# Kernel optimization log

Hardware: AMD Instinct MI355X
Metric: run time of the kernel (lower is better)

## Reference

```python
import jax, jax.numpy as jnp
import numpy as np

X_DIM = 64
Y_DIM = 64
U_DIM = 64
BATCH = 32
SEQ_LEN = 2048
DT = 1.0 / 1024.0
EPS = 1e-4


def setup_inputs() -> dict:
    key = jax.random.key(0)
    k_y, k_a, k_c = jax.random.split(key, 3)
    y = jax.random.normal(k_y, (BATCH, SEQ_LEN, Y_DIM), dtype=jnp.float32)
    # parameters, matching the module's initialization (small noise added to A/C for generality)
    A = jnp.diag(-0.01 * (jnp.arange(X_DIM, dtype=jnp.float32) + 1.0)) \
        + 0.001 * jax.random.normal(k_a, (X_DIM, X_DIM), dtype=jnp.float32)
    B = jnp.eye(X_DIM, U_DIM, dtype=jnp.float32) * 0.1
    C = 0.1 * jax.random.normal(k_c, (Y_DIM, X_DIM), dtype=jnp.float32)
    L_Q = jnp.eye(X_DIM, dtype=jnp.float32) * 0.316
    L_R = jnp.eye(U_DIM, dtype=jnp.float32) * 0.316
    L_V = jnp.eye(Y_DIM, dtype=jnp.float32)
    L_Q_proc = jnp.eye(X_DIM, dtype=jnp.float32) * 0.1
    x0_mean = jnp.zeros((X_DIM,), dtype=jnp.float32)
    P0 = jnp.eye(X_DIM, dtype=jnp.float32) * 0.1
    return {"y": y, "A": A, "B": B, "C": C, "L_Q": L_Q, "L_R": L_R,
            "L_V": L_V, "L_Q_proc": L_Q_proc, "x0_mean": x0_mean, "P0": P0}


def _riccati_step(S, H, n):
    # Euler step of the augmented Hamiltonian flow; P = V @ U^{-1}
    S_new = S + DT * (H @ S)
    U, V = S_new[:n], S_new[n:]
    X = V @ jnp.linalg.inv(U)
    return X, S_new


def _forward(y, A, B, C, L_Q, L_R, L_V, L_Q_proc, x0_mean, P0):
    n = A.shape[0]
    u_dim = B.shape[1]
    y_dim = C.shape[0]
    batch, seq_len, _ = y.shape

    Q = L_Q @ L_Q.T
    R = L_R @ L_R.T
    V = L_V @ L_V.T
    Q_proc = L_Q_proc @ L_Q_proc.T

    # normalize observations (torch.std is unbiased -> ddof=1)
    y_mean = y.mean(axis=(0, 1), keepdims=True)
    y_std = y.std(axis=(0, 1), keepdims=True, ddof=1)
    yn = (y - y_mean) / (y_std + EPS)

    # --- LQR Riccati recursion: P_seq, K_seq (sequential scan over time) ---
    R_inv_reg = jnp.linalg.inv(R + EPS * jnp.eye(u_dim, dtype=R.dtype))
    H_care = jnp.block([[A, -B @ jnp.linalg.inv(R) @ B.T],
                        [-Q, -A.T]])  # augmented Hamiltonian (2n, 2n)

    def lqr_step(S, _):
        X, S_new = _riccati_step(S, H_care, n)
        P = 0.5 * (X + X.T)
        K = R_inv_reg @ (B.T @ P)  # (u_dim, n)
        return S_new, (P, K)

    S0 = jnp.concatenate([jnp.eye(n, dtype=Q.dtype), Q], axis=0)  # P0 = Q
    _, (P_seq, K_seq) = jax.lax.scan(lqr_step, S0, None, length=seq_len)

    # --- Kalman filter (sequential scan, data-dependent per-step linear algebra) ---
    V_reg = V + EPS * jnp.eye(y_dim, dtype=V.dtype)
    V_chol = jnp.linalg.cholesky(V_reg)
    log_det_V = 2.0 * jnp.sum(jnp.log(jnp.diagonal(V_chol)))
    Z = jnp.zeros((n, n), dtype=A.dtype)
    LOG_2PI = jnp.log(2.0 * jnp.pi).astype(A.dtype)

    def kf_step(carry, inp):
        x_t, S, ll = carry
        K_t, y_t = inp  # (u_dim, n), (batch, y_dim)
        A_eff = A - B @ K_t
        x_pred = x_t + DT * (x_t @ A_eff.T)  # (batch, n)
        H_t = jnp.block([[A_eff, Q_proc], [Z, -A_eff.T]])
        P_new, S = _riccati_step(S, H_t, n)
        P_pred = 0.5 * (P_new + P_new.T)
        residual = y_t - x_pred @ C.T  # (batch, y_dim)
        CtP = C @ P_pred  # (y_dim, n)
        Sm = CtP @ C.T + V
        S_inv = jnp.linalg.inv(Sm + EPS * jnp.eye(y_dim, dtype=Sm.dtype))
        Kg = CtP.T @ S_inv  # (n, y_dim)
        x_new = x_pred + residual @ Kg.T
        quad = jnp.sum(residual * (residual @ S_inv.T))  # sum_b r^T S_inv r
        ll = ll - 0.5 * (quad + log_det_V + y_dim * LOG_2PI)
        return (x_new, S, ll), x_new

    S0_kf = jnp.concatenate([jnp.eye(n, dtype=P0.dtype), P0], axis=0)
    x0 = jnp.broadcast_to(x0_mean, (batch, n))
    y_t_major = jnp.swapaxes(yn, 0, 1)  # (T, B, y_dim)
    (_, _, ll), x_filt_t = jax.lax.scan(kf_step, (x0, S0_kf, jnp.float32(0.0)),
                                        (K_seq, y_t_major))
    x_filt = jnp.swapaxes(x_filt_t, 0, 1)  # (B, T, n)
    log_likelihood = ll / seq_len

    # controls, prediction, quadratic costs (fully vectorized)
    u_seq = -jnp.einsum('tux,btx->btu', K_seq, x_filt)
    y_pred = x_filt @ C.T
    x_cost = jnp.einsum('btx,xz,btz->b', x_filt, Q, x_filt)
    u_cost = jnp.einsum('btu,uv,btv->b', u_seq, R, u_seq)
    control_cost = jnp.mean(x_cost + u_cost)
    return log_likelihood, control_cost, x_filt, u_seq, y_pred, yn


def reference(y, A, B, C, L_Q, L_R, L_V, L_Q_proc, x0_mean, P0):
    return _forward(y, A, B, C, L_Q, L_R, L_V, L_Q_proc, x0_mean, P0)
```

## Files before the change

### kernel.cpp

```cpp
#include <hip/hip_runtime.h>
#include <math.h>

#define XD 64
#define SEQL 2048
#define NB 32
#define DT_C  (1.0f/1024.0f)
#define EPS_C 1e-4f
#define LD 68
#define LOG2PI 1.8378770664093453f
#define CHUNK 8
#define NCH 256

#define OFF_PARTIAL 0u
#define OFF_MEAN    32768u
#define OFF_STD     32832u
#define OFF_Q       32896u
#define OFF_R       36992u
#define OFF_VM      41088u
#define OFF_QP      45184u
#define OFF_RIREG   49280u
#define OFF_LOGDET  53376u
#define OFF_CHAIN   53440u
#define OFF_POW     250048u
#define OFF_BOUNDS  1298624u
#define OFF_K       1568960u
#define OFF_AEFF    9957568u
#define OFF_UV      18346176u
#define OFF_G       35123392u
#define OFF_B       43512000u
#define OFF_OPS2    OFF_UV
#define OFF_OPS3G   47706304u
#define OFF_OPS3B   49803456u
#define OFF_SB2     50852032u
#define OFF_XB      52949184u
#define OFF_QUAD    53473472u
#define OFF_COST    53475520u
#define OFF_BRI     53541056u

#define OOFF_XF 2
#define OOFF_U  4194306
#define OOFF_YP 8388610
#define OOFF_YN 12582914

template<int KD>
__device__ __forceinline__ void mmNN(int t, float* __restrict__ out, int ldo,
    const float* __restrict__ A, int lda, const float* __restrict__ B, int ldb,
    const float* __restrict__ addC = nullptr, int ldc = 0, float alpha = 1.0f)
{
  const int r0 = (t >> 4) << 2, c0 = (t & 15) << 2;
  float acc[4][4] = {};
  for (int k = 0; k < KD; k += 4) {
    float a_[4][4];
    #pragma unroll
    for (int i = 0; i < 4; ++i) {
      const float4 x = *(const float4*)&A[(r0+i)*lda + k];
      a_[i][0]=x.x; a_[i][1]=x.y; a_[i][2]=x.z; a_[i][3]=x.w;
    }
    #pragma unroll
    for (int kk = 0; kk < 4; ++kk) {
      const float4 bv = *(const float4*)&B[(k+kk)*ldb + c0];
      #pragma unroll
      for (int i = 0; i < 4; ++i) {
        const float a = a_[i][kk];
        acc[i][0] += a*bv.x; acc[i][1] += a*bv.y; acc[i][2] += a*bv.z; acc[i][3] += a*bv.w;
      }
    }
  }
  #pragma unroll
  for (int i = 0; i < 4; ++i)
    #pragma unroll
    for (int j = 0; j < 4; ++j) {
      float v = alpha*acc[i][j];
      if (addC) v += addC[(r0+i)*ldc + (c0+j)];
      out[(r0+i)*ldo + (c0+j)] = v;
    }
}

template<int KD>
__device__ __forceinline__ void mmTA(int t, float* __restrict__ out, int ldo,
    const float* __restrict__ A, int lda, const float* __restrict__ B, int ldb,
    const float* __restrict__ addC = nullptr, int ldc = 0, float alpha = 1.0f)
{
  const int r0 = (t >> 4) << 2, c0 = (t & 15) << 2;
  float acc[4][4] = {};
  for (int k = 0; k < KD; k += 4) {
    #pragma unroll
    for (int kk = 0; kk < 4; ++kk) {
      const float4 av4 = *(const float4*)&A[(k+kk)*lda + r0];
      const float4 bv4 = *(const float4*)&B[(k+kk)*ldb + c0];
      const float av[4] = {av4.x, av4.y, av4.z, av4.w};
      const float bv[4] = {bv4.x, bv4.y, bv4.z, bv4.w};
      #pragma unroll
      for (int i = 0; i < 4; ++i)
        #pragma unroll
        for (int j = 0; j < 4; ++j)
          acc[i][j] += av[i]*bv[j];
    }
  }
  #pragma unroll
  for (int i = 0; i < 4; ++i)
    #pragma unroll
    for (int j = 0; j < 4; ++j) {
      float v = alpha*acc[i][j];
      if (addC) v += addC[(r0+i)*ldc + (c0+j)];
      out[(r0+i)*ldo + (c0+j)] = v;
    }
}

template<int KD>
__device__ __forceinline__ void mmTB(int t, float* __restrict__ out, int ldo,
    const float* __restrict__ A, int lda, const float* __restrict__ B, int ldb,
    const float* __restrict__ addC = nullptr, int ldc = 0, float alpha = 1.0f)
{
  const int r0 = (t >> 4) << 2, c0 = (t & 15) << 2;
  float acc[4][4] = {};
  for (int k = 0; k < KD; k += 4) {
    float a_[4][4], b_[4][4];
    #pragma unroll
    for (int i = 0; i < 4; ++i) {
      const float4 x = *(const float4*)&A[(r0+i)*lda + k];
      a_[i][0]=x.x; a_[i][1]=x.y; a_[i][2]=x.z; a_[i][3]=x.w;
    }
    #pragma unroll
    for (int j = 0; j < 4; ++j) {
      const float4 x = *(const float4*)&B[(c0+j)*ldb + k];
      b_[j][0]=x.x; b_[j][1]=x.y; b_[j][2]=x.z; b_[j][3]=x.w;
    }
    #pragma unroll
    for (int i = 0; i < 4; ++i)
      #pragma unroll
      for (int j = 0; j < 4; ++j)
        acc[i][j] += a_[i][0]*b_[j][0] + a_[i][1]*b_[j][1] + a_[i][2]*b_[j][2] + a_[i][3]*b_[j][3];
  }
  #pragma unroll
  for (int i = 0; i < 4; ++i)
    #pragma unroll
    for (int j = 0; j < 4; ++j) {
      float v = alpha*acc[i][j];
      if (addC) v += addC[(r0+i)*ldc + (c0+j)];
      out[(r0+i)*ldo + (c0+j)] = v;
    }
}

__device__ __forceinline__ void symTile(int t, float* __restrict__ outb, const float* __restrict__ X)
{
  const int r0 = (t >> 4) << 2, c0 = (t & 15) << 2;
  float xa[4][4], xb[4][4];
  #pragma unroll
  for (int i = 0; i < 4; ++i) {
    const float4 u = *(const float4*)&X[(r0+i)*LD + c0];
    xa[i][0]=u.x; xa[i][1]=u.y; xa[i][2]=u.z; xa[i][3]=u.w;
    const float4 v = *(const float4*)&X[(c0+i)*LD + r0];
    xb[i][0]=v.x; xb[i][1]=v.y; xb[i][2]=v.z; xb[i][3]=v.w;
  }
  #pragma unroll
  for (int i = 0; i < 4; ++i) {
    float4 o;
    o.x = 0.5f*(xa[i][0] + xb[0][i]);
    o.y = 0.5f*(xa[i][1] + xb[1][i]);
    o.z = 0.5f*(xa[i][2] + xb[2][i]);
    o.w = 0.5f*(xa[i][3] + xb[3][i]);
    *(float4*)&outb[(r0+i)*LD + c0] = o;
  }
}

template<int KD>
__device__ __forceinline__ void mm32NN(int t, float* __restrict__ out, int ldo,
    const float* __restrict__ A, int lda, const float* __restrict__ B, int ldb,
    const float* __restrict__ addC = nullptr, int ldc = 0, float alpha = 1.0f)
{
  const int r0 = (t >> 4) << 1, c0 = (t & 15) << 2;
  float acc[2][4] = {};
  for (int k = 0; k < KD; k += 4) {
    float a_[2][4];
    #pragma unroll
    for (int i = 0; i < 2; ++i) {
      const float4 x = *(const float4*)&A[(r0+i)*lda + k];
      a_[i][0]=x.x; a_[i][1]=x.y; a_[i][2]=x.z; a_[i][3]=x.w;
    }
    #pragma unroll
    for (int kk = 0; kk < 4; ++kk) {
      const float4 bv = *(const float4*)&B[(k+kk)*ldb + c0];
      #pragma unroll
      for (int i = 0; i < 2; ++i) {
        const float a = a_[i][kk];
        acc[i][0] += a*bv.x; acc[i][1] += a*bv.y; acc[i][2] += a*bv.z; acc[i][3] += a*bv.w;
      }
    }
  }
  #pragma unroll
  for (int i = 0; i < 2; ++i)
    #pragma unroll
    for (int j = 0; j < 4; ++j) {
      float v = alpha*acc[i][j];
      if (addC) v += addC[(r0+i)*ldc + (c0+j)];
      out[(r0+i)*ldo + (c0+j)] = v;
    }
}

template<int KD>
__device__ __forceinline__ void mm32TB(int t, float* __restrict__ out, int ldo,
    const float* __restrict__ A, size_t lda, const float* __restrict__ B, int ldb,
    const float* __restrict__ addC = nullptr, size_t ldc = 0, float alpha = 1.0f)
{
  const int r0 = (t >> 4) << 1, c0 = (t & 15) << 2;
  float acc[2][4] = {};
  for (int k = 0; k < KD; k += 4) {
    float a_[2][4], b_[4][4];
    #pragma unroll
    for (int i = 0; i < 2; ++i) {
      const float4 x = *(const float4*)&A[(size_t)(r0+i)*lda + k];
      a_[i][0]=x.x; a_[i][1]=x.y; a_[i][2]=x.z; a_[i][3]=x.w;
    }
    #pragma unroll
    for (int j = 0; j < 4; ++j) {
      const float4 x = *(const float4*)&B[(c0+j)*ldb + k];
      b_[j][0]=x.x; b_[j][1]=x.y; b_[j][2]=x.z; b_[j][3]=x.w;
    }
    #pragma unroll
    for (int i = 0; i < 2; ++i)
      #pragma unroll
      for (int j = 0; j < 4; ++j)
        acc[i][j] += a_[i][0]*b_[j][0] + a_[i][1]*b_[j][1] + a_[i][2]*b_[j][2] + a_[i][3]*b_[j][3];
  }
  #pragma unroll
  for (int i = 0; i < 2; ++i)
    #pragma unroll
    for (int j = 0; j < 4; ++j) {
      float v = alpha*acc[i][j];
      if (addC) v += addC[(size_t)(r0+i)*ldc + (c0+j)];
      out[(r0+i)*ldo + (c0+j)] = v;
    }
}

__device__ __forceinline__ void gj64(int t, float* __restrict__ Am, float* __restrict__ R)
{
  const int r = t >> 2;
  const int c0 = (t & 3) << 4;
  for (int k = 0; k < 64; ++k) {
    __syncthreads();
    const float pv = Am[k*LD + k];
    const float f = Am[r*LD + k] / pv;
    if (r != k) {
      #pragma unroll
      for (int c = 0; c < 16; c += 4) {
        float4 ak = *(const float4*)&Am[k*LD + c0 + c];
        float4 ar = *(float4*)&Am[r*LD + c0 + c];
        ar.x -= f*ak.x; ar.y -= f*ak.y; ar.z -= f*ak.z; ar.w -= f*ak.w;
        *(float4*)&Am[r*LD + c0 + c] = ar;
        float4 rk = *(const float4*)&R[k*LD + c0 + c];
        float4 rr = *(float4*)&R[r*LD + c0 + c];
        rr.x -= f*rk.x; rr.y -= f*rk.y; rr.z -= f*rk.z; rr.w -= f*rk.w;
        *(float4*)&R[r*LD + c0 + c] = rr;
      }
    }
  }
  __syncthreads();
  const float dinv = 1.0f / Am[r*LD + r];
  #pragma unroll
  for (int c = 0; c < 16; c += 4) {
    float4 rr = *(float4*)&R[r*LD + c0 + c];
    rr.x *= dinv; rr.y *= dinv; rr.z *= dinv; rr.w *= dinv;
    *(float4*)&R[r*LD + c0 + c] = rr;
  }
  __syncthreads();
}

__device__ __forceinline__ void gji8(int t, float* __restrict__ Am)
{
  const int r  = t >> 2;
  const int c0 = (t & 3) << 4;
  const int pj = (t >> 4) & 7;
  const int c4 = (t & 15) << 2;
  const int lane = t & 63;
  const int li = lane >> 3, lj = lane & 7;
  for (int kb = 0; kb < 8; ++kb) {
    const int K = kb << 3;
    __syncthreads();
    const bool inK = ((unsigned)(r - K)) < 8u;
    float4 f0 = make_float4(0.f,0.f,0.f,0.f), f1 = f0;
    if (!inK) {
      f0 = *(const float4*)&Am[r*LD + K];
      f1 = *(const float4*)&Am[r*LD + K + 4];
    }
    float a = Am[(K+li)*LD + K + lj];
    float w = (li == lj) ? 1.0f : 0.0f;
    #pragma unroll
    for (int p = 0; p < 8; ++p) {
      const float pv  = __shfl(a, p*8 + p, 64);
      const float pvr = __builtin_amdgcn_rcpf(pv);
      const float aip = __shfl(a, li*8 + p, 64);
      const float apj = __shfl(a, p*8 + lj, 64);
      const float wpj = __shfl(w, p*8 + lj, 64);
      const float fi  = aip * pvr;
      if (li == p) { a *= pvr; w *= pvr; }
      else         { a -= fi * apj; w -= fi * wpj; }
    }
    float wrow[8];
    #pragma unroll
    for (int m = 0; m < 8; ++m) wrow[m] = __shfl(w, pj*8 + m, 64);
    float4 acc = make_float4(0.f,0.f,0.f,0.f);
    if (t < 128) {
      #pragma unroll
      for (int m = 0; m < 8; ++m) {
        const float4 rv = *(const float4*)&Am[(K+m)*LD + c4];
        acc.x += wrow[m]*rv.x; acc.y += wrow[m]*rv.y; acc.z += wrow[m]*rv.z; acc.w += wrow[m]*rv.w;
      }
      const unsigned dp = (unsigned)(c4 - K);
      if (dp < 8u) acc = make_float4(wrow[dp], wrow[dp+1], wrow[dp+2], wrow[dp+3]);
    }
    __syncthreads();
    if (t < 128) *(float4*)&Am[(K+pj)*LD + c4] = acc;
    __syncthreads();
    if (!inK) {
      const float fj[8] = {f0.x, f0.y, f0.z, f0.w, f1.x, f1.y, f1.z, f1.w};
      #pragma unroll
      for (int c = 0; c < 16; c += 4) {
        const int cab = c0 + c;
        const bool isPiv = ((unsigned)(cab - K)) < 8u;
        float4 v = isPiv ? make_float4(0.f,0.f,0.f,0.f) : *(float4*)&Am[r*LD + cab];
        #pragma unroll
        for (int j = 0; j < 8; ++j) {
          const float4 p4 = *(const float4*)&Am[(K+j)*LD + cab];
          v.x -= fj[j]*p4.x; v.y -= fj[j]*p4.y; v.z -= fj[j]*p4.z; v.w -= fj[j]*p4.w;
        }
        *(float4*)&Am[r*LD + cab] = v;
      }
    }
  }
  __syncthreads();
}


__global__ __launch_bounds__(256) void k_stats(const float* __restrict__ y, float* __restrict__ ws)
{
  __shared__ float sbuf[4][128];
  const int t = threadIdx.x, blk = blockIdx.x;
  const int d = t & 63, g = t >> 6;
  float s = 0.f, s2 = 0.f;
  for (int r = g; r < 256; r += 4) {
    const float v = y[(size_t)(blk*256 + r)*64 + d];
    s += v; s2 += v*v;
  }
  sbuf[g][d] = s; sbuf[g][64+d] = s2;
  __syncthreads();
  if (t < 128) ws[OFF_PARTIAL + (size_t)blk*128 + t] = sbuf[0][t]+sbuf[1][t]+sbuf[2][t]+sbuf[3][t];
}

__global__ __launch_bounds__(256) void k_setup(
    const float* __restrict__ A, const float* __restrict__ Bi,
    const float* __restrict__ LQ, const float* __restrict__ LR,
    const float* __restrict__ LV, const float* __restrict__ LQp,
    float* __restrict__ ws)
{
  __shared__ float b1[64*LD], b2[64*LD], b3[64*LD], b4[64*LD], bQ[64*LD];
  __shared__ float sred[128];
  const int t = threadIdx.x;

  if (t < 128) {
    float acc = 0.f;
    for (int p = 0; p < 256; ++p) acc += ws[OFF_PARTIAL + (size_t)p*128 + t];
    sred[t] = acc;
  }
  __syncthreads();
  if (t < 64) {
    const float mean = sred[t] * (1.0f/65536.0f);
    const float var = (sred[64+t] - 65536.0f*mean*mean) * (1.0f/65535.0f);
    ws[OFF_MEAN + t] = mean;
    ws[OFF_STD + t] = sqrtf(var);
  }

  mmTB<64>(t, bQ, LD, LQ, 64, LQ, 64);
  mmTB<64>(t, b3, LD, LR, 64, LR, 64);
  mmTB<64>(t, ws+OFF_VM, 64, LV, 64, LV, 64);
  mmTB<64>(t, ws+OFF_QP, 64, LQp, 64, LQp, 64);
  __syncthreads();
  for (int idx = t; idx < 4096; idx += 256) {
    const int r = idx>>6, c = idx&63;
    ws[OFF_Q + idx] = bQ[r*LD+c];
    ws[OFF_R + idx] = b3[r*LD+c];
    b1[r*LD+c] = b3[r*LD+c] + ((r==c)?EPS_C:0.f);
    b2[r*LD+c] = (r==c)?1.f:0.f;
  }
  gj64(t, b1, b2);
  mmNN<64>(t, b4, LD, Bi, 64, b2, LD);
  __syncthreads();
  for (int idx = t; idx < 4096; idx += 256) {
    ws[OFF_RIREG + idx] = b2[(idx>>6)*LD+(idx&63)];
    ws[OFF_BRI + idx]   = b4[(idx>>6)*LD+(idx&63)];
  }
  __syncthreads();
  for (int idx = t; idx < 4096; idx += 256) {
    const int r = idx>>6, c = idx&63;
    b1[r*LD+c] = b3[r*LD+c];
    b2[r*LD+c] = (r==c)?1.f:0.f;
  }
  gj64(t, b1, b2);
  mmTB<64>(t, b3, LD, b2, LD, Bi, 64);
  __syncthreads();
  mmNN<64>(t, b4, LD, Bi, 64, b3, LD);
  mmTB<64>(t, b1, LD, LV, 64, LV, 64);
  __syncthreads();
  if (t < 64) b1[t*LD+t] += EPS_C;
  {
    const int r = t >> 2, c0 = (t & 3) << 4;
    float lsum = 0.f;
    for (int k = 0; k < 64; ++k) {
      __syncthreads();
      const float pv = b1[k*LD+k];
      lsum += logf(pv);
      const float f = b1[r*LD+k] / pv;
      if (r != k) {
        #pragma unroll
        for (int c = 0; c < 16; c += 4) {
          float4 ak = *(const float4*)&b1[k*LD+c0+c];
          float4 ar = *(float4*)&b1[r*LD+c0+c];
          ar.x -= f*ak.x; ar.y -= f*ak.y; ar.z -= f*ak.z; ar.w -= f*ak.w;
          *(float4*)&b1[r*LD+c0+c] = ar;
        }
      }
    }
    if (t == 0) ws[OFF_LOGDET] = lsum;
  }
  __syncthreads();
  float* M0 = ws + OFF_CHAIN;
  for (int idx = t; idx < 16384; idx += 256) {
    const int i = idx >> 7, j = idx & 127;
    float v;
    if (i < 64) v = (j < 64) ? (((i==j)?1.f:0.f) + DT_C*A[i*64+j]) : (-DT_C*b4[i*LD + (j-64)]);
    else        v = (j < 64) ? (-DT_C*bQ[(i-64)*LD + j]) : (((i==j)?1.f:0.f) - DT_C*A[(j-64)*64 + (i-64)]);
    M0[idx] = v;
  }
  for (int idx = t; idx < 16384; idx += 256) {
    const int i = idx >> 7, j = idx & 127;
    ws[OFF_POW + idx] = (i==j)?1.f:0.f;
  }
  for (int idx = t; idx < 8192; idx += 256) {
    const int i = idx >> 6, j = idx & 63;
    ws[OFF_BOUNDS + idx] = (i < 64) ? ((i==j)?1.f:0.f) : bQ[(i-64)*LD + j];
  }
}

__global__ __launch_bounds__(256) void k_yn(const float* __restrict__ y, const float* __restrict__ ws, float* __restrict__ out)
{
  const size_t i0 = ((size_t)blockIdx.x*256 + threadIdx.x)*4;
  const int d = (int)(i0 & 63);
  const float4 v = *(const float4*)&y[i0];
  const float4 m = *(const float4*)&ws[OFF_MEAN + d];
  const float4 s = *(const float4*)&ws[OFF_STD + d];
  float* o = out + OOFF_YN + i0;
  o[0] = (v.x - m.x)/(s.x + EPS_C);
  o[1] = (v.y - m.y)/(s.y + EPS_C);
  o[2] = (v.z - m.z)/(s.z + EPS_C);
  o[3] = (v.w - m.w)/(s.w + EPS_C);
}

__global__ __launch_bounds__(256) void k_sq(const float* __restrict__ src, float* __restrict__ dst)
{
  const int t = threadIdx.x;
  const int r = blockIdx.x*8 + (t >> 5);
  const int c0 = (t & 31) << 2;
  float acc[4] = {0.f,0.f,0.f,0.f};
  for (int k = 0; k < 128; k += 4) {
    const float4 a4 = *(const float4*)&src[r*128 + k];
    const float av[4] = {a4.x, a4.y, a4.z, a4.w};
    #pragma unroll
    for (int kk = 0; kk < 4; ++kk) {
      const float4 bv = *(const float4*)&src[(k+kk)*128 + c0];
      acc[0] += av[kk]*bv.x; acc[1] += av[kk]*bv.y; acc[2] += av[kk]*bv.z; acc[3] += av[kk]*bv.w;
    }
  }
  float4 o; o.x=acc[0]; o.y=acc[1]; o.z=acc[2]; o.w=acc[3];
  *(float4*)&dst[r*128 + c0] = o;
}

__global__ __launch_bounds__(256) void k_powbounds(const float* __restrict__ chain, float* __restrict__ ws, int level)
{
  const int nbp = 4 << level;
  const int t = threadIdx.x;
  if ((int)blockIdx.x < nbp) {
    const float* chainj = chain + (size_t)level*16384;
    float* powt = ws + OFF_POW;
    const int i = blockIdx.x >> 2, sub = blockIdx.x & 3;
    const float* Bm = powt + (size_t)i*16384;
    float* D = powt + (size_t)(i + (1<<level))*16384;
    const int r0 = sub*32 + ((t >> 4) << 1);
    const int c0 = (t & 15) << 3;
    float acc[2][8] = {};
    for (int k = 0; k < 128; k += 4) {
      float a_[2][4];
      {
        const float4 x = *(const float4*)&chainj[r0*128 + k];
        a_[0][0]=x.x; a_[0][1]=x.y; a_[0][2]=x.z; a_[0][3]=x.w;
        const float4 y2 = *(const float4*)&chainj[(r0+1)*128 + k];
        a_[1][0]=y2.x; a_[1][1]=y2.y; a_[1][2]=y2.z; a_[1][3]=y2.w;
      }
      #pragma unroll
      for (int kk = 0; kk < 4; ++kk) {
        const float4 b0 = *(const float4*)&Bm[(k+kk)*128 + c0];
        const float4 b1v = *(const float4*)&Bm[(k+kk)*128 + c0 + 4];
        #pragma unroll
        for (int i2 = 0; i2 < 2; ++i2) {
          const float a = a_[i2][kk];
          acc[i2][0] += a*b0.x; acc[i2][1] += a*b0.y; acc[i2][2] += a*b0.z; acc[i2][3] += a*b0.w;
          acc[i2][4] += a*b1v.x; acc[i2][5] += a*b1v.y; acc[i2][6] += a*b1v.z; acc[i2][7] += a*b1v.w;
        }
      }
    }
    #pragma unroll
    for (int i2 = 0; i2 < 2; ++i2)
      #pragma unroll
      for (int j = 0; j < 8; ++j)
        D[(r0+i2)*128 + c0 + j] = acc[i2][j];
  } else {
    const int bb = blockIdx.x - nbp;
    const int kb = bb >> 1, sub = bb & 1;
    const int dsti = kb + (1 << level);
    if (dsti > 32) return;
    const float* chainp = chain + (size_t)(6+level)*16384;
    const float* S = ws + OFF_BOUNDS + (size_t)kb*8192;
    float* D = ws + OFF_BOUNDS + (size_t)dsti*8192;
    const int r0 = sub*64 + ((t >> 4) << 2);
    const int c0 = (t & 15) << 2;
    float acc[4][4] = {};
    for (int k = 0; k < 128; k += 4) {
      float a_[4][4];
      #pragma unroll
      for (int i = 0; i < 4; ++i) {
        const float4 x = *(const float4*)&chainp[(r0+i)*128 + k];
        a_[i][0]=x.x; a_[i][1]=x.y; a_[i][2]=x.z; a_[i][3]=x.w;
      }
      #pragma unroll
      for (int kk = 0; kk < 4; ++kk) {
        const float4 bv = *(const float4*)&S[(k+kk)*64 + c0];
        #pragma unroll
        for (int i = 0; i < 4; ++i) {
          const float a = a_[i][kk];
          acc[i][0] += a*bv.x; acc[i][1] += a*bv.y; acc[i][2] += a*bv.z; acc[i][3] += a*bv.w;
        }
      }
    }
    #pragma unroll
    for (int i = 0; i < 4; ++i)
      #pragma unroll
      for (int j = 0; j < 4; ++j)
        D[(r0+i)*64 + c0 + j] = acc[i][j];
  }
}

__global__ __launch_bounds__(256) void k_lqr(const float* __restrict__ Ain, const float* __restrict__ Bin, float* __restrict__ ws)
{
  __shared__ float b1[64*LD], b2[64*LD], b3[64*LD];
  const int t = threadIdx.x, tt = blockIdx.x;
  const int tp1 = tt + 1, kc = tp1 >> 6, rr = tp1 & 63;
  const float* Mr = ws + OFF_POW + (size_t)rr*16384;
  const float* SB = ws + OFF_BOUNDS + (size_t)kc*8192;
  mmNN<128>(t, b1, LD, Mr, 128, SB, 64);
  mmNN<128>(t, b3, LD, Mr + 8192, 128, SB, 64);
  gji8(t, b1);
  mmNN<64>(t, b2, LD, b3, LD, b1, LD);
  __syncthreads();
  symTile(t, b3, b2);
  __syncthreads();
  mmTA<64>(t, b1, LD, Bin, 64, b3, LD);
  __syncthreads();
  mmNN<64>(t, b2, LD, ws+OFF_RIREG, 64, b1, LD);
  mmNN<64>(t, b3, LD, ws+OFF_BRI, 64, b1, LD);
  __syncthreads();
  float* Kout = ws + OFF_K + (size_t)tt*4096;
  float* Ae   = ws + OFF_AEFF + (size_t)tt*4096;
  for (int idx = t; idx < 4096; idx += 256) {
    const int p = (idx>>6)*LD + (idx&63);
    Kout[idx] = b2[p];
    Ae[idx]   = Ain[idx] - b3[p];
  }
}

__global__ __launch_bounds__(1024) void k_ops2(const float* __restrict__ ws_aeff, const float* __restrict__ ws_qp, float* __restrict__ dstE)
{
  __shared__ float E[64*LD], W[64*LD], F[64*LD], T1[64*LD], T2[64*LD], T3[64*LD], T4[64*LD];
  const int t = threadIdx.x, c = blockIdx.x, g = t >> 8, tl = t & 255;
  for (int idx = t; idx < 4096; idx += 1024) {
    const int r = idx>>6, cc = idx&63; const float id = (r==cc)?1.f:0.f;
    E[r*LD+cc] = id; W[r*LD+cc] = 0.f; F[r*LD+cc] = id;
  }
  __syncthreads();
  for (int s = 0; s < CHUNK; ++s) {
    const float* Ae = ws_aeff + ((size_t)c*CHUNK + s)*4096;
    if (g == 0)      mmNN<64>(tl, T1, LD, Ae, 64, E, LD);
    else if (g == 1) mmNN<64>(tl, T2, LD, Ae, 64, W, LD);
    else if (g == 2) mmNN<64>(tl, T3, LD, ws_qp, 64, F, LD);
    else             mmTA<64>(tl, T4, LD, Ae, 64, F, LD);
    __syncthreads();
    for (int idx = t; idx < 4096; idx += 1024) {
      const int p = (idx>>6)*LD + (idx&63);
      E[p] += DT_C*T1[p];
      W[p] += DT_C*(T2[p] + T3[p]);
      F[p] -= DT_C*T4[p];
    }
    __syncthreads();
  }
  float* dst = dstE + (size_t)c*12288;
  for (int idx = t; idx < 4096; idx += 1024) {
    const int p = (idx>>6)*LD + (idx&63);
    dst[idx] = E[p]; dst[4096+idx] = W[p]; dst[8192+idx] = F[p];
  }
}

__global__ __launch_bounds__(1024) void k_scan2(const float* __restrict__ src, float* __restrict__ dst, int s)
{
  __shared__ float t1[64*LD], t2[64*LD];
  const int i = blockIdx.x, t = threadIdx.x, g = t>>8, tl = t&255;
  const float* si = src + (size_t)i*12288;
  float* di = dst + (size_t)i*12288;
  if (i < s) {
    for (int idx = t; idx < 12288; idx += 1024) di[idx] = si[idx];
    return;
  }
  const float* sj = src + (size_t)(i-s)*12288;
  if (g == 0)      mmNN<64>(tl, di, 64, si, 64, sj, 64);
  else if (g == 1) mmNN<64>(tl, t1, LD, si, 64, sj+4096, 64);
  else if (g == 2) mmNN<64>(tl, t2, LD, si+4096, 64, sj+8192, 64);
  else             mmNN<64>(tl, di+8192, 64, si+8192, 64, sj+8192, 64);
  __syncthreads();
  for (int idx = t; idx < 4096; idx += 1024) {
    const int p = (idx>>6)*LD + (idx&63);
    di[4096+idx] = t1[p] + t2[p];
  }
}

__global__ __launch_bounds__(256) void k_sb2(const float* __restrict__ phi, const float* __restrict__ P0, float* __restrict__ ws)
{
  const int c = blockIdx.x, t = threadIdx.x;
  float* D = ws + OFF_SB2 + (size_t)c*8192;
  if (c == 0) {
    for (int idx = t; idx < 4096; idx += 256) {
      const int r = idx>>6, cc = idx&63;
      D[idx] = (r==cc)?1.f:0.f;
      D[4096+idx] = P0[idx];
    }
    return;
  }
  const float* ph = phi + (size_t)(c-1)*12288;
  mmNN<64>(t, D, 64, ph+4096, 64, P0, 64, ph, 64);
  mmNN<64>(t, D+4096, 64, ph+8192, 64, P0, 64);
}

__global__ __launch_bounds__(1024) void k_uvwalk(const float* __restrict__ ws_aeff, const float* __restrict__ ws_qp,
    const float* __restrict__ ws_sb2, float* __restrict__ ws_uv)
{
  __shared__ float U[64*LD], V[64*LD], T1[64*LD], T2[64*LD], T3[64*LD];
  const int c = blockIdx.x, t = threadIdx.x, g = t>>8, tl = t&255;
  const float* S = ws_sb2 + (size_t)c*8192;
  for (int idx = t; idx < 4096; idx += 1024) {
    const int p = (idx>>6)*LD + (idx&63);
    U[p] = S[idx]; V[p] = S[4096+idx];
  }
  __syncthreads();
  for (int s = 0; s < CHUNK; ++s) {
    const size_t tt = (size_t)c*CHUNK + s;
    const float* Ae = ws_aeff + tt*4096;
    if (g == 0)      mmNN<64>(tl, T1, LD, Ae, 64, U, LD);
    else if (g == 1) mmNN<64>(tl, T2, LD, ws_qp, 64, V, LD);
    else if (g == 2) mmTA<64>(tl, T3, LD, Ae, 64, V, LD);
    __syncthreads();
    float* O = ws_uv + tt*8192;
    for (int idx = t; idx < 4096; idx += 1024) {
      const int p = (idx>>6)*LD + (idx&63);
      const float un = U[p] + DT_C*(T1[p] + T2[p]);
      const float vn = V[p] - DT_C*T3[p];
      U[p] = un; V[p] = vn;
      O[idx] = un; O[4096+idx] = vn;
    }
    __syncthreads();
  }
}

__global__ __launch_bounds__(256) void k_kfper(const float* __restrict__ Cin, const float* __restrict__ outyn, float* __restrict__ ws)
{
  __shared__ float b1[64*LD], b2[64*LD], b3[64*LD];
  const int t = threadIdx.x, tt = blockIdx.x;
  float* base = ws + OFF_UV + (size_t)tt*8192;
  for (int idx = t; idx < 4096; idx += 256) {
    const int r = idx>>6, c = idx&63;
    b1[r*LD+c] = base[idx];
    b3[r*LD+c] = base[4096+idx];
  }
  gji8(t, b1);
  mmNN<64>(t, b2, LD, b3, LD, b1, LD);
  __syncthreads();
  symTile(t, b3, b2);
  __syncthreads();
  mmNN<64>(t, b1, LD, Cin, 64, b3, LD);
  __syncthreads();
  mmTB<64>(t, b2, LD, b1, LD, Cin, 64, ws+OFF_VM, 64);
  __syncthreads();
  if (t < 64) b2[t*LD+t] += EPS_C;
  gji8(t, b2);
  for (int idx = t; idx < 4096; idx += 256) base[4096+idx] = b2[(idx>>6)*LD+(idx&63)];
  mmTA<64>(t, b3, LD, b1, LD, b2, LD);
  __syncthreads();
  for (int idx = t; idx < 4096; idx += 256) base[idx] = b3[(idx>>6)*LD+(idx&63)];
  mmNN<64>(t, b2, LD, b3, LD, Cin, 64);
  __syncthreads();
  const float* Ae = ws + OFF_AEFF + (size_t)tt*4096;
  float* Gg = ws + OFF_G + (size_t)tt*4096;
  {
    const int r0 = (t>>4)<<2, cg0 = (t&15)<<2;
    float acc[4][4] = {};
    for (int k = 0; k < 64; k += 4) {
      float a_[4][4];
      #pragma unroll
      for (int kk = 0; kk < 4; ++kk) {
        const float4 x = *(const float4*)&Ae[(k+kk)*64 + r0];
        a_[kk][0]=x.x; a_[kk][1]=x.y; a_[kk][2]=x.z; a_[kk][3]=x.w;
      }
      float yv[4][4];
      #pragma unroll
      for (int j = 0; j < 4; ++j) {
        const float4 z4 = *(const float4*)&b2[(cg0+j)*LD + k];
        yv[j][0] = -z4.x; yv[j][1] = -z4.y; yv[j][2] = -z4.z; yv[j][3] = -z4.w;
        const int dk = (cg0+j) - k;
        if (dk >= 0 && dk < 4) yv[j][dk] += 1.0f;
      }
      #pragma unroll
      for (int kk = 0; kk < 4; ++kk)
        #pragma unroll
        for (int i = 0; i < 4; ++i) {
          const float a = a_[kk][i];
          #pragma unroll
          for (int j = 0; j < 4; ++j) acc[i][j] += a * yv[j][kk];
        }
    }
    #pragma unroll
    for (int i = 0; i < 4; ++i)
      #pragma unroll
      for (int j = 0; j < 4; ++j) {
        const int rw = r0+i, cw = cg0+j;
        const float Yij = ((rw==cw)?1.f:0.f) - b2[cw*LD + rw];
        b1[rw*LD+cw] = Yij + DT_C*acc[i][j];
      }
  }
  __syncthreads();
  for (int idx = t; idx < 4096; idx += 256) Gg[idx] = b1[(idx>>6)*LD+(idx&63)];
  mm32TB<64>(t, b2, LD, outyn + (size_t)tt*64, (size_t)131072, b3, LD);
  __syncthreads();
  float* Bout = ws + OFF_B + (size_t)tt*2048;
  for (int idx = t; idx < 2048; idx += 256) Bout[idx] = b2[(idx>>6)*LD+(idx&63)];
}

__global__ __launch_bounds__(1024) void k_ops3(const float* __restrict__ ws_g, const float* __restrict__ ws_b,
    float* __restrict__ dG, float* __restrict__ dB)
{
  __shared__ float Gc[64*LD], TG[64*LD], bc[NB*LD], Tb[NB*LD];
  const int t = threadIdx.x, c = blockIdx.x, g = t >> 8, tl = t & 255;
  for (int idx = t; idx < 4096; idx += 1024) {
    const int r = idx>>6, cc = idx&63;
    Gc[r*LD+cc] = (r==cc)?1.f:0.f;
  }
  for (int idx = t; idx < 2048; idx += 1024) bc[(idx>>6)*LD+(idx&63)] = 0.f;
  __syncthreads();
  for (int s = 0; s < CHUNK; ++s) {
    const size_t tt = (size_t)c*CHUNK + s;
    const float* Gt = ws_g + tt*4096;
    if (g == 0)      mmNN<64>(tl, TG, LD, Gc, LD, Gt, 64);
    else if (g == 1) mm32NN<64>(tl, Tb, LD, bc, LD, Gt, 64);
    __syncthreads();
    for (int idx = t; idx < 4096; idx += 1024) {
      const int p = (idx>>6)*LD + (idx&63);
      Gc[p] = TG[p];
    }
    const float* bt = ws_b + tt*2048;
    for (int idx = t; idx < 2048; idx += 1024) {
      const int p = (idx>>6)*LD + (idx&63);
      bc[p] = Tb[p] + bt[idx];
    }
    __syncthreads();
  }
  for (int idx = t; idx < 4096; idx += 1024) dG[(size_t)c*4096 + idx] = Gc[(idx>>6)*LD+(idx&63)];
  for (int idx = t; idx < 2048; idx += 1024) dB[(size_t)c*2048 + idx] = bc[(idx>>6)*LD+(idx&63)];
}

__global__ __launch_bounds__(512) void k_scan3(const float* __restrict__ sG, const float* __restrict__ sB,
    float* __restrict__ dG, float* __restrict__ dB, int s)
{
  const int i = blockIdx.x, t = threadIdx.x, g = t>>8, tl = t&255;
  if (i < s) {
    for (int idx = t; idx < 4096; idx += 512) dG[(size_t)i*4096+idx] = sG[(size_t)i*4096+idx];
    for (int idx = t; idx < 2048; idx += 512) dB[(size_t)i*2048+idx] = sB[(size_t)i*2048+idx];
    return;
  }
  const float* Ge = sG + (size_t)(i-s)*4096;
  const float* Gl = sG + (size_t)i*4096;
  if (g == 0) mmNN<64>(tl, dG + (size_t)i*4096, 64, Ge, 64, Gl, 64);
  else        mm32NN<64>(tl, dB + (size_t)i*2048, 64, sB + (size_t)(i-s)*2048, 64, Gl, 64,
                         sB + (size_t)i*2048, 64);
}

__global__ __launch_bounds__(256) void k_xb(const float* __restrict__ phiG, const float* __restrict__ phiB,
    const float* __restrict__ x0, float* __restrict__ ws)
{
  __shared__ float v[64];
  const int c = blockIdx.x, t = threadIdx.x;
  float* D = ws + OFF_XB + (size_t)c*2048;
  if (c == 0) {
    for (int idx = t; idx < 2048; idx += 256) D[idx] = x0[idx&63];
    return;
  }
  const float* G = phiG + (size_t)(c-1)*4096;
  const float* b = phiB + (size_t)(c-1)*2048;
  if (t < 64) {
    float acc = 0.f;
    for (int k = 0; k < 64; ++k) acc += x0[k]*G[k*64 + t];
    v[t] = acc;
  }
  __syncthreads();
  for (int idx = t; idx < 2048; idx += 256) D[idx] = v[idx&63] + b[idx];
}

__global__ __launch_bounds__(256) void k_xwalk(const float* __restrict__ ws_g, const float* __restrict__ ws_b,
    const float* __restrict__ ws_xb, float* __restrict__ outx)
{
  __shared__ float x[NB*LD], xn[NB*LD];
  const int c = blockIdx.x, t = threadIdx.x;
  const float* X0 = ws_xb + (size_t)c*2048;
  for (int idx = t; idx < 2048; idx += 256) x[(idx>>6)*LD+(idx&63)] = X0[idx];
  __syncthreads();
  for (int s = 0; s < CHUNK; ++s) {
    const size_t tt = (size_t)c*CHUNK + s;
    mm32NN<64>(t, xn, LD, x, LD, ws_g + tt*4096, 64, ws_b + tt*2048, 64);
    __syncthreads();
    for (int idx = t; idx < 2048; idx += 256) {
      const int i = idx>>6, d = idx&63;
      const float val = xn[i*LD+d];
      x[i*LD+d] = val;
      outx[(size_t)i*131072 + tt*64 + d] = val;
    }
    __syncthreads();
  }
}

__global__ __launch_bounds__(256) void k_final(const float* __restrict__ Cin, const float* __restrict__ x0,
    const float* __restrict__ outx, const float* __restrict__ outyn,
    float* __restrict__ outu, float* __restrict__ outyp, float* __restrict__ ws)
{
  __shared__ float xc[NB*LD], z[NB*LD], t1[NB*LD], t2[NB*LD];
  __shared__ float red4[4];
  const int tt = blockIdx.x, t = threadIdx.x;
  for (int idx = t; idx < 2048; idx += 256) {
    const int i = idx>>6, d = idx&63;
    xc[i*LD+d] = outx[(size_t)i*131072 + (size_t)tt*64 + d];
    z[i*LD+d]  = (tt == 0) ? x0[d] : outx[(size_t)i*131072 + (size_t)(tt-1)*64 + d];
  }
  __syncthreads();
  mm32TB<64>(t, t1, LD, xc, LD, ws + OFF_K + (size_t)tt*4096, 64, nullptr, 0, -1.0f);
  mm32TB<64>(t, t2, LD, xc, LD, Cin, 64);
  __syncthreads();
  for (int idx = t; idx < 2048; idx += 256) {
    const int i = idx>>6, d = idx&63;
    outu[(size_t)i*131072 + (size_t)tt*64 + d]  = t1[i*LD+d];
    outyp[(size_t)i*131072 + (size_t)tt*64 + d] = t2[i*LD+d];
  }
  __syncthreads();
  mm32NN<64>(t, t2, LD, xc, LD, ws + OFF_Q, 64);
  __syncthreads();
  const int i_ = t >> 3, lane8 = t & 7;
  float cpart = 0.f;
  for (int d = lane8; d < 64; d += 8) cpart += t2[i_*LD+d]*xc[i_*LD+d];
  __syncthreads();
  mm32NN<64>(t, t2, LD, t1, LD, ws + OFF_R, 64);
  __syncthreads();
  for (int d = lane8; d < 64; d += 8) cpart += t2[i_*LD+d]*t1[i_*LD+d];
  cpart += __shfl_down(cpart, 4, 8);
  cpart += __shfl_down(cpart, 2, 8);
  cpart += __shfl_down(cpart, 1, 8);
  if (lane8 == 0) ws[OFF_COST + (size_t)tt*32 + i_] = cpart;
  __syncthreads();
  mm32TB<64>(t, t2, LD, z, LD, ws + OFF_AEFF + (size_t)tt*4096, 64, z, LD, DT_C);
  __syncthreads();
  mm32TB<64>(t, t1, LD, t2, LD, Cin, 64, outyn + (size_t)tt*64, (size_t)131072, -1.0f);
  __syncthreads();
  mm32TB<64>(t, z, LD, t1, LD, ws + OFF_UV + (size_t)tt*8192 + 4096, 64);
  __syncthreads();
  float q = 0.f;
  for (int idx = t; idx < 2048; idx += 256) {
    const int p = (idx>>6)*LD + (idx&63);
    q += t1[p]*z[p];
  }
  q += __shfl_down(q, 32); q += __shfl_down(q, 16); q += __shfl_down(q, 8);
  q += __shfl_down(q, 4);  q += __shfl_down(q, 2);  q += __shfl_down(q, 1);
  if ((t & 63) == 0) red4[t>>6] = q;
  __syncthreads();
  if (t == 0) ws[OFF_QUAD + tt] = red4[0]+red4[1]+red4[2]+red4[3];
}

__global__ __launch_bounds__(256) void k_scalars(const float* __restrict__ ws, float* __restrict__ out)
{
  __shared__ float red[256];
  const int t = threadIdx.x;
  float q = 0.f;
  for (int i = t; i < 2048; i += 256) q += ws[OFF_QUAD + i];
  red[t] = q;
  __syncthreads();
  for (int s = 128; s > 0; s >>= 1) { if (t < s) red[t] += red[t+s]; __syncthreads(); }
  const float quadsum = red[0];
  __syncthreads();
  {
    const int b = t & 31, chunk = t >> 5;
    float a = 0.f;
    for (int j = 0; j < 256; ++j) a += ws[OFF_COST + (size_t)(chunk*256 + j)*32 + b];
    red[t] = a;
  }
  __syncthreads();
  if (t < 32) {
    float a = 0.f;
    for (int ch = 0; ch < 8; ++ch) a += red[ch*32 + t];
    red[t] = a;
  }
  __syncthreads();
  if (t == 0) {
    float cc = 0.f;
    for (int b = 0; b < 32; ++b) cc += red[b];
    out[1] = cc / 32.0f;
    const float ld = ws[OFF_LOGDET];
    out[0] = -0.5f*(quadsum + 2048.0f*(ld + 64.0f*LOG2PI)) / 2048.0f;
  }
}

extern "C" void kernel_launch(void* const* d_in, const int* in_sizes, int n_in,
                              void* d_out, int out_size, void* d_ws, size_t ws_size,
                              hipStream_t stream)
{
  (void)in_sizes; (void)n_in; (void)out_size; (void)ws_size;
  const float* y   = (const float*)d_in[0];
  const float* A   = (const float*)d_in[1];
  const float* Bi  = (const float*)d_in[2];
  const float* C   = (const float*)d_in[3];
  const float* LQ  = (const float*)d_in[4];
  const float* LR  = (const float*)d_in[5];
  const float* LV  = (const float*)d_in[6];
  const float* LQp = (const float*)d_in[7];
  const float* x0  = (const float*)d_in[8];
  const float* P0  = (const float*)d_in[9];
  float* out = (float*)d_out;
  float* ws  = (float*)d_ws;

  k_stats<<<256, 256, 0, stream>>>(y, ws);
  k_setup<<<1, 256, 0, stream>>>(A, Bi, LQ, LR, LV, LQp, ws);
  k_yn<<<4096, 256, 0, stream>>>(y, ws, out);

  for (int j = 1; j <= 11; ++j)
    k_sq<<<16, 256, 0, stream>>>(ws + OFF_CHAIN + (size_t)(j-1)*16384, ws + OFF_CHAIN + (size_t)j*16384);
  for (int j = 0; j <= 5; ++j)
    k_powbounds<<<6 << j, 256, 0, stream>>>(ws + OFF_CHAIN, ws, j);

  k_lqr<<<2048, 256, 0, stream>>>(A, Bi, ws);

  k_ops2<<<NCH, 1024, 0, stream>>>(ws + OFF_AEFF, ws + OFF_QP, ws + OFF_OPS2);
  {
    float* pa = ws + OFF_OPS2;
    float* pb = pa + (size_t)NCH*12288;
    float* src = pa; float* dst = pb;
    for (int s = 1; s < NCH; s <<= 1) {
      k_scan2<<<NCH, 1024, 0, stream>>>(src, dst, s);
      float* tmp = src; src = dst; dst = tmp;
    }
    k_sb2<<<NCH, 256, 0, stream>>>(src, P0, ws);
  }
  k_uvwalk<<<NCH, 1024, 0, stream>>>(ws + OFF_AEFF, ws + OFF_QP, ws + OFF_SB2, ws + OFF_UV);
  k_kfper<<<2048, 256, 0, stream>>>(C, out + OOFF_YN, ws);

  k_ops3<<<NCH, 1024, 0, stream>>>(ws + OFF_G, ws + OFF_B, ws + OFF_OPS3G, ws + OFF_OPS3B);
  {
    float* ga = ws + OFF_OPS3G; float* gb = ga + (size_t)NCH*4096;
    float* ba = ws + OFF_OPS3B; float* bb = ba + (size_t)NCH*2048;
    float *gs = ga, *gd = gb, *bs = ba, *bd = bb;
    for (int s = 1; s < NCH; s <<= 1) {
      k_scan3<<<NCH, 512, 0, stream>>>(gs, bs, gd, bd, s);
      float* t1p = gs; gs = gd; gd = t1p;
      float* t2p = bs; bs = bd; bd = t2p;
    }
    k_xb<<<NCH, 256, 0, stream>>>(gs, bs, x0, ws);
  }
  k_xwalk<<<NCH, 256, 0, stream>>>(ws + OFF_G, ws + OFF_B, ws + OFF_XB, out + OOFF_XF);

  k_final<<<2048, 256, 0, stream>>>(C, x0, out + OOFF_XF, out + OOFF_YN, out + OOFF_U, out + OOFF_YP, ws);
  k_scalars<<<1, 256, 0, stream>>>(ws, out);
}
```

Baseline: 2.276 ms.

## Replace per-step power-matrix LQR state with chunked Euler walk from chunk boundaries

The old kernel rebuilt each time step's Hamiltonian state by multiplying a 128x128 power matrix by a boundary state, one 128x128x64 product per step. The new path computes one starting state per chunk of 8 steps (k_sbl), then steps forward with explicit Euler updates split across four thread groups (k_lqrwalk), and stores U and V for every step. The per-step kernel then only loads the stored state. This cuts the heavy per-step matmul work but adds two launches, a serial walk inside each chunk, and extra global traffic for the stored states, and the numerics shift slightly because of Euler accumulation.

```diff
diff --git a/kernel.cpp b/kernel.cpp
--- a/kernel.cpp
+++ b/kernel.cpp
@@ -36,6 +36,7 @@
 #define OFF_QUAD    53473472u
 #define OFF_COST    53475520u
 #define OFF_BRI     53541056u
+#define OFF_BRB     53545152u
 
 #define OOFF_XF 2
 #define OOFF_U  4194306
@@ -401,6 +402,8 @@
   mmNN<64>(t, b4, LD, Bi, 64, b3, LD);
   mmTB<64>(t, b1, LD, LV, 64, LV, 64);
   __syncthreads();
+  for (int idx = t; idx < 4096; idx += 256)
+    ws[OFF_BRB + idx] = b4[(idx>>6)*LD+(idx&63)];
   if (t < 64) b1[t*LD+t] += EPS_C;
   {
     const int r = t >> 2, c0 = (t & 3) << 4;
@@ -548,15 +551,80 @@
   }
 }
 
-__global__ __launch_bounds__(256) void k_lqr(const float* __restrict__ Ain, const float* __restrict__ Bin, float* __restrict__ ws)
+__global__ __launch_bounds__(256) void k_sbl(const float* __restrict__ ws_pow, const float* __restrict__ ws_bounds, float* __restrict__ dst)
+{
+  const int c = blockIdx.x >> 1, sub = blockIdx.x & 1;
+  const float* Mr = ws_pow + (size_t)((c & 7) << 3)*16384;
+  const float* S  = ws_bounds + (size_t)(c >> 3)*8192;
+  float* D = dst + (size_t)c*8192;
+  const int t = threadIdx.x;
+  const int r0 = sub*64 + ((t >> 4) << 2);
+  const int c0 = (t & 15) << 2;
+  float acc[4][4] = {};
+  for (int k = 0; k < 128; k += 4) {
+    float a_[4][4];
+    #pragma unroll
+    for (int i = 0; i < 4; ++i) {
+      const float4 x = *(const float4*)&Mr[(r0+i)*128 + k];
+      a_[i][0]=x.x; a_[i][1]=x.y; a_[i][2]=x.z; a_[i][3]=x.w;
+    }
+    #pragma unroll
+    for (int kk = 0; kk < 4; ++kk) {
+      const float4 bv = *(const float4*)&S[(k+kk)*64 + c0];
+      #pragma unroll
+      for (int i = 0; i < 4; ++i) {
+        const float a = a_[i][kk];
+        acc[i][0] += a*bv.x; acc[i][1] += a*bv.y; acc[i][2] += a*bv.z; acc[i][3] += a*bv.w;
+      }
+    }
+  }
+  #pragma unroll
+  for (int i = 0; i < 4; ++i)
+    #pragma unroll
+    for (int j = 0; j < 4; ++j)
+      D[(r0+i)*64 + c0 + j] = acc[i][j];
+}
+
+__global__ __launch_bounds__(1024) void k_lqrwalk(const float* __restrict__ Ain, const float* __restrict__ ws_q,
+    const float* __restrict__ ws_brb, const float* __restrict__ ws_sbl, float* __restrict__ ws_uv)
+{
+  __shared__ float U[64*LD], V[64*LD], T1[64*LD], T2[64*LD], T3[64*LD], T4[64*LD];
+  const int c = blockIdx.x, t = threadIdx.x, g = t>>8, tl = t&255;
+  const float* S = ws_sbl + (size_t)c*8192;
+  for (int idx = t; idx < 4096; idx += 1024) {
+    const int p = (idx>>6)*LD + (idx&63);
+    U[p] = S[idx]; V[p] = S[4096+idx];
+  }
+  __syncthreads();
+  for (int s = 0; s < CHUNK; ++s) {
+    if (g == 0)      mmNN<64>(tl, T1, LD, Ain, 64, U, LD);
+    else if (g == 1) mmNN<64>(tl, T2, LD, ws_brb, 64, V, LD);
+    else if (g == 2) mmNN<64>(tl, T3, LD, ws_q, 64, U, LD);
+    else             mmTA<64>(tl, T4, LD, Ain, 64, V, LD);
+    __syncthreads();
+    const size_t tt = (size_t)c*CHUNK + s;
+    float* O = ws_uv + tt*8192;
+    for (int idx = t; idx < 4096; idx += 1024) {
+      const int p = (idx>>6)*LD + (idx&63);
+      const float un = U[p] + DT_C*(T1[p] - T2[p]);
+      const float vn = V[p] - DT_C*(T3[p] + T4[p]);
+      U[p] = un; V[p] = vn;
+      O[idx] = un; O[4096+idx] = vn;
+    }
+    __syncthreads();
+  }
+}
+
+__global__ __launch_bounds__(256) void k_lqrper(const float* __restrict__ Ain, const float* __restrict__ Bin, float* __restrict__ ws)
 {
   __shared__ float b1[64*LD], b2[64*LD], b3[64*LD];
   const int t = threadIdx.x, tt = blockIdx.x;
-  const int tp1 = tt + 1, kc = tp1 >> 6, rr = tp1 & 63;
-  const float* Mr = ws + OFF_POW + (size_t)rr*16384;
-  const float* SB = ws + OFF_BOUNDS + (size_t)kc*8192;
-  mmNN<128>(t, b1, LD, Mr, 128, SB, 64);
-  mmNN<128>(t, b3, LD, Mr + 8192, 128, SB, 64);
+  const float* base = ws + OFF_UV + (size_t)tt*8192;
+  for (int idx = t; idx < 4096; idx += 256) {
+    const int r = idx>>6, c = idx&63;
+    b1[r*LD+c] = base[idx];
+    b3[r*LD+c] = base[4096+idx];
+  }
   gji8(t, b1);
   mmNN<64>(t, b2, LD, b3, LD, b1, LD);
   __syncthreads();
@@ -954,7 +1022,9 @@
   for (int j = 0; j <= 5; ++j)
     k_powbounds<<<6 << j, 256, 0, stream>>>(ws + OFF_CHAIN, ws, j);
 
-  k_lqr<<<2048, 256, 0, stream>>>(A, Bi, ws);
+  k_sbl<<<512, 256, 0, stream>>>(ws + OFF_POW, ws + OFF_BOUNDS, ws + OFF_SB2);
+  k_lqrwalk<<<NCH, 1024, 0, stream>>>(A, ws + OFF_Q, ws + OFF_BRB, ws + OFF_SB2, ws + OFF_UV);
+  k_lqrper<<<2048, 256, 0, stream>>>(A, Bi, ws);
 
   k_ops2<<<NCH, 1024, 0, stream>>>(ws + OFF_AEFF, ws + OFF_QP, ws + OFF_OPS2);
   {
```

New measurement: 2.296 ms. About the same (+0.9%).
